# Optimization experiments

Measured on AMD Instinct MI355X. Metric: run time of the kernel, lower is better.

## Reference

```python
import jax, jax.numpy as jnp
import numpy as np

IN_CH = 64
HIDDEN_CH = 256

def setup_inputs() -> dict:
    key = jax.random.key(0)
    k = jax.random.split(key, 8)
    za = jax.random.normal(k[0], (8, 256, IN_CH), dtype=jnp.float32)
    zb = jax.random.normal(k[1], (8, 256, IN_CH), dtype=jnp.float32)
    # 1x1 conv weights stored as (out_ch, in_ch); biases zero per torch init
    w0 = jax.random.normal(k[2], (HIDDEN_CH, IN_CH), dtype=jnp.float32) * 0.05
    b0 = jnp.zeros((HIDDEN_CH,), dtype=jnp.float32)
    w1 = jax.random.normal(k[3], (HIDDEN_CH, HIDDEN_CH), dtype=jnp.float32) * 0.05
    b1 = jnp.zeros((HIDDEN_CH,), dtype=jnp.float32)
    w2 = jax.random.normal(k[4], (1, HIDDEN_CH), dtype=jnp.float32) * 0.05
    b2 = jnp.zeros((1,), dtype=jnp.float32)
    return {"za": za, "zb": zb, "w0": w0, "b0": b0, "w1": w1, "b1": b1, "w2": w2, "b2": b2}

def _leaky_relu(x):
    return jnp.where(x >= 0, x, 0.01 * x)  # torch LeakyReLU default slope

def reference(za, zb, w0, b0, w1, b1, w2, b2):
    # z_dif: (N, A, B, C) pairwise broadcast difference (channel-last; 1x1 conv = per-pixel linear)
    z_dif = za[:, :, None, :] - zb[:, None, :, :]
    y = _leaky_relu(jnp.einsum('nabc,hc->nabh', z_dif, w0) + b0)
    y = _leaky_relu(jnp.einsum('nabh,gh->nabg', y, w1) + b1)
    y = jax.nn.sigmoid(jnp.einsum('nabh,oh->nabo', y, w2) + b2)
    return y[..., 0]  # (N, A, B)
```

## Files before the change

### kernel.cpp

```cpp
#include <hip/hip_runtime.h>


typedef float f32x16 __attribute__((ext_vector_type(16)));
typedef short bf16x8 __attribute__((ext_vector_type(8)));

static __device__ __forceinline__ unsigned short f32_to_bf16(float f) {
    unsigned int u = __float_as_uint(f);
    u += 0x7FFFu + ((u >> 16) & 1u);
    return (unsigned short)(u >> 16);
}
static __device__ __forceinline__ float bf16_to_f32(unsigned short s) {
    return __uint_as_float(((unsigned int)s) << 16);
}

__global__ __launch_bounds__(256) void pack_uv_kernel(
    const float* __restrict__ za, const float* __restrict__ zb,
    const float* __restrict__ w0, const float* __restrict__ b0,
    unsigned short* __restrict__ upack, unsigned short* __restrict__ vpack) {
  int bid = blockIdx.x;
  int which = bid >> 11;
  int nr = bid & 2047;
  int n = nr >> 8, r = nr & 255;
  const float* z = (which ? zb : za) + nr * 64;
  __shared__ float zrow[64];
  int tid = threadIdx.x;
  if (tid < 64) zrow[tid] = z[tid];
  __syncthreads();
  int h = tid;
  const float* w0r = w0 + h * 64;
  float acc = 0.f;
#pragma unroll
  for (int c = 0; c < 64; c += 4) {
    float4 w = *reinterpret_cast<const float4*>(w0r + c);
    acc += w.x * zrow[c] + w.y * zrow[c + 1] + w.z * zrow[c + 2] + w.w * zrow[c + 3];
  }
  if (which == 0) {
    acc += b0[h];
    upack[nr * 256 + h] = f32_to_bf16(acc);
  } else {
    int bblock = r >> 5, lcol = r & 31;
    int kiter = h >> 4, rem = h & 15, half = rem >> 3, j = rem & 7;
    int lane = half * 32 + lcol;
    vpack[(((n * 8 + bblock) * 16 + kiter) * 64 + lane) * 8 + j] = f32_to_bf16(acc);
  }
}

__global__ __launch_bounds__(256) void pack_w1_kernel(
    const float* __restrict__ w1, unsigned short* __restrict__ w1pk) {
  int id = blockIdx.x * 256 + threadIdx.x;
  int g = id >> 8, h = id & 255;
  float val = w1[id];
  int nb = g >> 5, lcol = g & 31;
  int kiter = h >> 4, rem = h & 15, half = rem >> 3, j = rem & 7;
  int lane = half * 32 + lcol;
  w1pk[((kiter * 8 + nb) * 64 + lane) * 8 + j] = f32_to_bf16(val);
}

__global__ __launch_bounds__(512, 2) void fused_main_kernel(
    const unsigned short* __restrict__ upack,
    const unsigned short* __restrict__ vpack,
    const unsigned short* __restrict__ w1pk,
    const float* __restrict__ b1, const float* __restrict__ w2,
    const float* __restrict__ b2, float* __restrict__ out) {
  __shared__ __align__(16) unsigned short lwb[32768];
  int bid = blockIdx.x;
  int n = bid >> 8;
  int tid = threadIdx.x;
  int wid = tid >> 6;
  int l = tid & 63;
  int l31 = l & 31, lh = l >> 5;

  f32x16 acc[8];
#pragma unroll
  for (int cf = 0; cf < 8; ++cf)
#pragma unroll
    for (int r = 0; r < 16; ++r) acc[cf][r] = 0.f;

  float b1v[8], w2v[8];
#pragma unroll
  for (int cf = 0; cf < 8; ++cf) {
    b1v[cf] = b1[cf * 32 + l31];
    w2v[cf] = w2[cf * 32 + l31];
  }

  const bf16x8* vp8 = reinterpret_cast<const bf16x8*>(vpack);
  const unsigned short* ub = upack + bid * 256;
  const bf16x8* w1p8 = reinterpret_cast<const bf16x8*>(w1pk);
  bf16x8* lwb8 = reinterpret_cast<bf16x8*>(lwb);

  int vbase = ((n * 8 + wid) * 16) * 64 + l;

  for (int khalf = 0; khalf < 2; ++khalf) {
    __syncthreads();
#pragma unroll
    for (int it = 0; it < 8; ++it) {
      int cid = it * 512 + tid;
      lwb8[cid] = w1p8[khalf * 4096 + cid];
    }
    __syncthreads();

    bf16x8 afrag[8];
#pragma unroll
    for (int kk = 0; kk < 8; ++kk) {
      int kiter = khalf * 8 + kk;
      bf16x8 vv = vp8[vbase + kiter * 64];
      bf16x8 uu = *reinterpret_cast<const bf16x8*>(ub + kiter * 16 + lh * 8);
#pragma unroll
      for (int j = 0; j < 8; ++j) {
        float d = bf16_to_f32((unsigned short)uu[j]) - bf16_to_f32((unsigned short)vv[j]);
        d = fmaxf(d, 0.01f * d);
        afrag[kk][j] = (short)f32_to_bf16(d);
      }
    }

#pragma unroll
    for (int kk = 0; kk < 8; ++kk) {
#pragma unroll
      for (int cf = 0; cf < 8; ++cf) {
        bf16x8 bfrag = lwb8[(kk * 8 + cf) * 64 + l];
        acc[cf] = __builtin_amdgcn_mfma_f32_32x32x16_bf16(afrag[kk], bfrag, acc[cf], 0, 0, 0);
      }
    }
  }

  float p[16];
#pragma unroll
  for (int r = 0; r < 16; ++r) p[r] = 0.f;
#pragma unroll
  for (int cf = 0; cf < 8; ++cf) {
#pragma unroll
    for (int r = 0; r < 16; ++r) {
      float h1 = acc[cf][r] + b1v[cf];
      h1 = fmaxf(h1, 0.01f * h1);
      p[r] += h1 * w2v[cf];
    }
  }
#pragma unroll
  for (int r = 0; r < 16; ++r) {
#pragma unroll
    for (int m = 1; m < 32; m <<= 1) p[r] += __shfl_xor(p[r], m, 64);
  }
  float b2v = b2[0];
  if (l31 == 0) {
    int obase = bid * 256 + wid * 32 + 4 * lh;
#pragma unroll
    for (int r = 0; r < 16; ++r) {
      int row = (r & 3) + 8 * (r >> 2);
      out[obase + row] = 1.f / (1.f + __expf(-(p[r] + b2v)));
    }
  }
}

extern "C" void kernel_launch(void* const* d_in, const int* in_sizes, int n_in,
                              void* d_out, int out_size, void* d_ws, size_t ws_size,
                              hipStream_t stream) {
  const float* za = (const float*)d_in[0];
  const float* zb = (const float*)d_in[1];
  const float* w0 = (const float*)d_in[2];
  const float* b0 = (const float*)d_in[3];
  const float* w1 = (const float*)d_in[4];
  const float* b1 = (const float*)d_in[5];
  const float* w2 = (const float*)d_in[6];
  const float* b2 = (const float*)d_in[7];
  float* out = (float*)d_out;

  char* ws = (char*)d_ws;
  unsigned short* upack = (unsigned short*)ws;
  unsigned short* vpack = (unsigned short*)(ws + (1u << 20));
  unsigned short* w1pk  = (unsigned short*)(ws + (2u << 20));

  pack_uv_kernel<<<4096, 256, 0, stream>>>(za, zb, w0, b0, upack, vpack);
  pack_w1_kernel<<<256, 256, 0, stream>>>(w1, w1pk);
  fused_main_kernel<<<2048, 512, 0, stream>>>(upack, vpack, w1pk, b1, w2, b2, out);
}
```

Measured before the change: 163.1 us.

## Process two A rows per block with full W1 in LDS via direct global-to-LDS loads

The main kernel now gives each 256-thread block two A rows and half the B columns, so every B fragment read from LDS feeds two MFMAs. All of W1 (128 KB) is staged into LDS at once using global_load_lds, with a 64 KB two-phase fallback if the larger allocation is refused. U and V are kept in fp32 and converted to bf16 only after the subtraction, which improves accuracy but doubles their global traffic. The pack kernel also computes the za and zb projections in one launch. The cost is one block per CU, which limits latency hiding, and higher register use from two accumulator sets.

```diff
diff --git a/kernel.cpp b/kernel.cpp
--- a/kernel.cpp
+++ b/kernel.cpp
@@ -5,44 +5,36 @@
 typedef short bf16x8 __attribute__((ext_vector_type(8)));
 
 static __device__ __forceinline__ unsigned short f32_to_bf16(float f) {
-    unsigned int u = __float_as_uint(f);
-    u += 0x7FFFu + ((u >> 16) & 1u);
-    return (unsigned short)(u >> 16);
-}
-static __device__ __forceinline__ float bf16_to_f32(unsigned short s) {
-    return __uint_as_float(((unsigned int)s) << 16);
+  unsigned int u = __float_as_uint(f);
+  u += 0x7FFFu + ((u >> 16) & 1u);
+  return (unsigned short)(u >> 16);
 }
 
 __global__ __launch_bounds__(256) void pack_uv_kernel(
     const float* __restrict__ za, const float* __restrict__ zb,
     const float* __restrict__ w0, const float* __restrict__ b0,
-    unsigned short* __restrict__ upack, unsigned short* __restrict__ vpack) {
-  int bid = blockIdx.x;
-  int which = bid >> 11;
-  int nr = bid & 2047;
+    float* __restrict__ upack, float* __restrict__ vpack) {
+  int nr = blockIdx.x;
   int n = nr >> 8, r = nr & 255;
-  const float* z = (which ? zb : za) + nr * 64;
-  __shared__ float zrow[64];
+  __shared__ float arow[64], brow[64];
   int tid = threadIdx.x;
-  if (tid < 64) zrow[tid] = z[tid];
+  if (tid < 64) arow[tid] = za[nr * 64 + tid];
+  else if (tid < 128) brow[tid - 64] = zb[nr * 64 + (tid - 64)];
   __syncthreads();
   int h = tid;
   const float* w0r = w0 + h * 64;
-  float acc = 0.f;
+  float ua = 0.f, vb = 0.f;
 #pragma unroll
   for (int c = 0; c < 64; c += 4) {
     float4 w = *reinterpret_cast<const float4*>(w0r + c);
-    acc += w.x * zrow[c] + w.y * zrow[c + 1] + w.z * zrow[c + 2] + w.w * zrow[c + 3];
+    ua += w.x * arow[c] + w.y * arow[c + 1] + w.z * arow[c + 2] + w.w * arow[c + 3];
+    vb += w.x * brow[c] + w.y * brow[c + 1] + w.z * brow[c + 2] + w.w * brow[c + 3];
   }
-  if (which == 0) {
-    acc += b0[h];
-    upack[nr * 256 + h] = f32_to_bf16(acc);
-  } else {
-    int bblock = r >> 5, lcol = r & 31;
-    int kiter = h >> 4, rem = h & 15, half = rem >> 3, j = rem & 7;
-    int lane = half * 32 + lcol;
-    vpack[(((n * 8 + bblock) * 16 + kiter) * 64 + lane) * 8 + j] = f32_to_bf16(acc);
-  }
+  upack[nr * 256 + h] = ua + b0[h];
+  int bblock = r >> 5, lcol = r & 31;
+  int kiter = h >> 4, rem = h & 15, half = rem >> 3, j = rem & 7;
+  int lane = half * 32 + lcol;
+  vpack[(((n * 8 + bblock) * 16 + kiter) * 64 + lane) * 8 + j] = vb;
 }
 
 __global__ __launch_bounds__(256) void pack_w1_kernel(
@@ -56,25 +48,29 @@
   w1pk[((kiter * 8 + nb) * 64 + lane) * 8 + j] = f32_to_bf16(val);
 }
 
-__global__ __launch_bounds__(512, 2) void fused_main_kernel(
-    const unsigned short* __restrict__ upack,
-    const unsigned short* __restrict__ vpack,
+template <int KCHUNK>
+__global__ __launch_bounds__(256, 1) void fused_main(
+    const float* __restrict__ upack, const float* __restrict__ vpack,
     const unsigned short* __restrict__ w1pk,
     const float* __restrict__ b1, const float* __restrict__ w2,
     const float* __restrict__ b2, float* __restrict__ out) {
-  __shared__ __align__(16) unsigned short lwb[32768];
+  extern __shared__ __align__(16) unsigned char lds_raw[];
   int bid = blockIdx.x;
   int n = bid >> 8;
+  int apair = (bid >> 1) & 127;
+  int bhalf = bid & 1;
+  int a0 = apair * 2, a1 = a0 + 1;
   int tid = threadIdx.x;
   int wid = tid >> 6;
   int l = tid & 63;
   int l31 = l & 31, lh = l >> 5;
+  int bblk = bhalf * 4 + wid;
 
-  f32x16 acc[8];
+  f32x16 acc0[8], acc1[8];
 #pragma unroll
   for (int cf = 0; cf < 8; ++cf)
 #pragma unroll
-    for (int r = 0; r < 16; ++r) acc[cf][r] = 0.f;
+    for (int r = 0; r < 16; ++r) { acc0[cf][r] = 0.f; acc1[cf][r] = 0.f; }
 
   float b1v[8], w2v[8];
 #pragma unroll
@@ -83,70 +79,88 @@
     w2v[cf] = w2[cf * 32 + l31];
   }
 
-  const bf16x8* vp8 = reinterpret_cast<const bf16x8*>(vpack);
-  const unsigned short* ub = upack + bid * 256;
-  const bf16x8* w1p8 = reinterpret_cast<const bf16x8*>(w1pk);
-  bf16x8* lwb8 = reinterpret_cast<bf16x8*>(lwb);
+  const bf16x8* lfrag = reinterpret_cast<const bf16x8*>(lds_raw);
+  const int nphase = 16 / KCHUNK;
 
-  int vbase = ((n * 8 + wid) * 16) * 64 + l;
-
-  for (int khalf = 0; khalf < 2; ++khalf) {
-    __syncthreads();
+  for (int ph = 0; ph < nphase; ++ph) {
+    if (ph) __syncthreads();
+    const unsigned char* gsrc =
+        reinterpret_cast<const unsigned char*>(w1pk) + ph * KCHUNK * 8192;
 #pragma unroll
-    for (int it = 0; it < 8; ++it) {
-      int cid = it * 512 + tid;
-      lwb8[cid] = w1p8[khalf * 4096 + cid];
+    for (int it = 0; it < KCHUNK * 2; ++it) {
+      int chunk = it * 4 + wid;
+      __builtin_amdgcn_global_load_lds(
+          (const __attribute__((address_space(1))) void*)(gsrc + chunk * 1024 + l * 16),
+          (__attribute__((address_space(3))) void*)(lds_raw + chunk * 1024),
+          16, 0, 0);
     }
     __syncthreads();
 
-    bf16x8 afrag[8];
+    const float* vb = vpack + ((size_t)((n * 8 + bblk) * 16 + ph * KCHUNK)) * 512 + l * 8;
+    const float* u0b = upack + (n * 256 + a0) * 256 + ph * KCHUNK * 16 + lh * 8;
+    const float* u1b = upack + (n * 256 + a1) * 256 + ph * KCHUNK * 16 + lh * 8;
+
 #pragma unroll
-    for (int kk = 0; kk < 8; ++kk) {
-      int kiter = khalf * 8 + kk;
-      bf16x8 vv = vp8[vbase + kiter * 64];
-      bf16x8 uu = *reinterpret_cast<const bf16x8*>(ub + kiter * 16 + lh * 8);
+    for (int kk = 0; kk < KCHUNK; ++kk) {
+      float4 vA = *reinterpret_cast<const float4*>(vb + kk * 512);
+      float4 vB = *reinterpret_cast<const float4*>(vb + kk * 512 + 4);
+      float4 uA0 = *reinterpret_cast<const float4*>(u0b + kk * 16);
+      float4 uA1 = *reinterpret_cast<const float4*>(u0b + kk * 16 + 4);
+      float4 uB0 = *reinterpret_cast<const float4*>(u1b + kk * 16);
+      float4 uB1 = *reinterpret_cast<const float4*>(u1b + kk * 16 + 4);
+      float vv[8] = {vA.x, vA.y, vA.z, vA.w, vB.x, vB.y, vB.z, vB.w};
+      float u0[8] = {uA0.x, uA0.y, uA0.z, uA0.w, uA1.x, uA1.y, uA1.z, uA1.w};
+      float u1[8] = {uB0.x, uB0.y, uB0.z, uB0.w, uB1.x, uB1.y, uB1.z, uB1.w};
+      bf16x8 af0, af1;
 #pragma unroll
       for (int j = 0; j < 8; ++j) {
-        float d = bf16_to_f32((unsigned short)uu[j]) - bf16_to_f32((unsigned short)vv[j]);
-        d = fmaxf(d, 0.01f * d);
-        afrag[kk][j] = (short)f32_to_bf16(d);
+        float d0 = u0[j] - vv[j];
+        d0 = fmaxf(d0, 0.01f * d0);
+        af0[j] = (short)f32_to_bf16(d0);
+        float d1 = u1[j] - vv[j];
+        d1 = fmaxf(d1, 0.01f * d1);
+        af1[j] = (short)f32_to_bf16(d1);
       }
-    }
-
-#pragma unroll
-    for (int kk = 0; kk < 8; ++kk) {
 #pragma unroll
       for (int cf = 0; cf < 8; ++cf) {
-        bf16x8 bfrag = lwb8[(kk * 8 + cf) * 64 + l];
-        acc[cf] = __builtin_amdgcn_mfma_f32_32x32x16_bf16(afrag[kk], bfrag, acc[cf], 0, 0, 0);
+        bf16x8 bf = lfrag[(kk * 8 + cf) * 64 + l];
+        acc0[cf] = __builtin_amdgcn_mfma_f32_32x32x16_bf16(af0, bf, acc0[cf], 0, 0, 0);
+        acc1[cf] = __builtin_amdgcn_mfma_f32_32x32x16_bf16(af1, bf, acc1[cf], 0, 0, 0);
       }
     }
   }
 
-  float p[16];
+  float p0[16], p1[16];
 #pragma unroll
-  for (int r = 0; r < 16; ++r) p[r] = 0.f;
+  for (int r = 0; r < 16; ++r) { p0[r] = 0.f; p1[r] = 0.f; }
 #pragma unroll
   for (int cf = 0; cf < 8; ++cf) {
 #pragma unroll
     for (int r = 0; r < 16; ++r) {
-      float h1 = acc[cf][r] + b1v[cf];
+      float h0 = acc0[cf][r] + b1v[cf];
+      h0 = fmaxf(h0, 0.01f * h0);
+      p0[r] += h0 * w2v[cf];
+      float h1 = acc1[cf][r] + b1v[cf];
       h1 = fmaxf(h1, 0.01f * h1);
-      p[r] += h1 * w2v[cf];
+      p1[r] += h1 * w2v[cf];
     }
   }
 #pragma unroll
   for (int r = 0; r < 16; ++r) {
 #pragma unroll
-    for (int m = 1; m < 32; m <<= 1) p[r] += __shfl_xor(p[r], m, 64);
+    for (int m = 1; m < 32; m <<= 1) {
+      p0[r] += __shfl_xor(p0[r], m, 64);
+      p1[r] += __shfl_xor(p1[r], m, 64);
+    }
   }
   float b2v = b2[0];
   if (l31 == 0) {
-    int obase = bid * 256 + wid * 32 + 4 * lh;
+    int bcol = bhalf * 128 + wid * 32 + 4 * lh;
 #pragma unroll
     for (int r = 0; r < 16; ++r) {
       int row = (r & 3) + 8 * (r >> 2);
-      out[obase + row] = 1.f / (1.f + __expf(-(p[r] + b2v)));
+      out[(n * 256 + a0) * 256 + bcol + row] = 1.f / (1.f + __expf(-(p0[r] + b2v)));
+      out[(n * 256 + a1) * 256 + bcol + row] = 1.f / (1.f + __expf(-(p1[r] + b2v)));
     }
   }
 }
@@ -165,11 +179,19 @@
   float* out = (float*)d_out;
 
   char* ws = (char*)d_ws;
-  unsigned short* upack = (unsigned short*)ws;
-  unsigned short* vpack = (unsigned short*)(ws + (1u << 20));
-  unsigned short* w1pk  = (unsigned short*)(ws + (2u << 20));
+  float* upack = (float*)ws;
+  float* vpack = (float*)(ws + (2u << 20));
+  unsigned short* w1pk = (unsigned short*)(ws + (4u << 20));
 
-  pack_uv_kernel<<<4096, 256, 0, stream>>>(za, zb, w0, b0, upack, vpack);
+  pack_uv_kernel<<<2048, 256, 0, stream>>>(za, zb, w0, b0, upack, vpack);
   pack_w1_kernel<<<256, 256, 0, stream>>>(w1, w1pk);
-  fused_main_kernel<<<2048, 512, 0, stream>>>(upack, vpack, w1pk, b1, w2, b2, out);
+
+  hipError_t e = hipFuncSetAttribute(
+      reinterpret_cast<const void*>(fused_main<16>),
+      hipFuncAttributeMaxDynamicSharedMemorySize, 131072);
+  if (e == hipSuccess) {
+    fused_main<16><<<2048, 256, 131072, stream>>>(upack, vpack, w1pk, b1, w2, b2, out);
+  } else {
+    fused_main<8><<<2048, 256, 65536, stream>>>(upack, vpack, w1pk, b1, w2, b2, out);
+  }
 }
```

Measured after the change: 166.7 us. 1.02x slower.

## Keep W1 in registers, switch to fp16 packed math, restructure main kernel tiling

Applied to the files above, without the earlier changes.

The main kernel now holds each wave's slice of W1 as fp16 MFMA fragments in registers for the whole block and loops over 32 rows of A. This replaces reloading W1 into shared memory per block. The pairwise difference and LeakyReLU are computed with packed fp16 vector ops instead of per-element bf16/fp32 conversions, and the bias is folded into the accumulator init. The u/v packing is merged into one launch with half the blocks. Risks are the heavy register use for the W1 fragments, a per-row __syncthreads for the cross-wave reduction, and a different numerical precision.

```diff
diff --git a/kernel.cpp b/kernel.cpp
--- a/kernel.cpp
+++ b/kernel.cpp
@@ -1,152 +1,128 @@
 #include <hip/hip_runtime.h>
+#include <hip/hip_fp16.h>
 
 
 typedef float f32x16 __attribute__((ext_vector_type(16)));
-typedef short bf16x8 __attribute__((ext_vector_type(8)));
-
-static __device__ __forceinline__ unsigned short f32_to_bf16(float f) {
-    unsigned int u = __float_as_uint(f);
-    u += 0x7FFFu + ((u >> 16) & 1u);
-    return (unsigned short)(u >> 16);
-}
-static __device__ __forceinline__ float bf16_to_f32(unsigned short s) {
-    return __uint_as_float(((unsigned int)s) << 16);
-}
+typedef _Float16 f16x8 __attribute__((ext_vector_type(8)));
 
 __global__ __launch_bounds__(256) void pack_uv_kernel(
     const float* __restrict__ za, const float* __restrict__ zb,
     const float* __restrict__ w0, const float* __restrict__ b0,
-    unsigned short* __restrict__ upack, unsigned short* __restrict__ vpack) {
-  int bid = blockIdx.x;
-  int which = bid >> 11;
-  int nr = bid & 2047;
+    _Float16* __restrict__ upack, _Float16* __restrict__ vpack) {
+  int nr = blockIdx.x;
   int n = nr >> 8, r = nr & 255;
-  const float* z = (which ? zb : za) + nr * 64;
-  __shared__ float zrow[64];
+  __shared__ float arow[64], brow[64];
   int tid = threadIdx.x;
-  if (tid < 64) zrow[tid] = z[tid];
+  if (tid < 64) arow[tid] = za[nr * 64 + tid];
+  else if (tid < 128) brow[tid - 64] = zb[nr * 64 + (tid - 64)];
   __syncthreads();
   int h = tid;
   const float* w0r = w0 + h * 64;
-  float acc = 0.f;
+  float ua = 0.f, vb = 0.f;
 #pragma unroll
   for (int c = 0; c < 64; c += 4) {
     float4 w = *reinterpret_cast<const float4*>(w0r + c);
-    acc += w.x * zrow[c] + w.y * zrow[c + 1] + w.z * zrow[c + 2] + w.w * zrow[c + 3];
+    ua += w.x * arow[c] + w.y * arow[c + 1] + w.z * arow[c + 2] + w.w * arow[c + 3];
+    vb += w.x * brow[c] + w.y * brow[c + 1] + w.z * brow[c + 2] + w.w * brow[c + 3];
   }
-  if (which == 0) {
-    acc += b0[h];
-    upack[nr * 256 + h] = f32_to_bf16(acc);
-  } else {
-    int bblock = r >> 5, lcol = r & 31;
-    int kiter = h >> 4, rem = h & 15, half = rem >> 3, j = rem & 7;
-    int lane = half * 32 + lcol;
-    vpack[(((n * 8 + bblock) * 16 + kiter) * 64 + lane) * 8 + j] = f32_to_bf16(acc);
-  }
+  upack[nr * 256 + h] = (_Float16)(ua + b0[h]);
+  int bblk = r >> 5, lcol = r & 31;
+  int kiter = h >> 4, rem = h & 15, lh = rem >> 3, j = rem & 7;
+  int lane = lh * 32 + lcol;
+  vpack[(((n * 8 + bblk) * 16 + kiter) * 64 + lane) * 8 + j] = (_Float16)vb;
 }
 
 __global__ __launch_bounds__(256) void pack_w1_kernel(
-    const float* __restrict__ w1, unsigned short* __restrict__ w1pk) {
+    const float* __restrict__ w1, _Float16* __restrict__ w1pk) {
   int id = blockIdx.x * 256 + threadIdx.x;
-  int g = id >> 8, h = id & 255;
-  float val = w1[id];
-  int nb = g >> 5, lcol = g & 31;
-  int kiter = h >> 4, rem = h & 15, half = rem >> 3, j = rem & 7;
-  int lane = half * 32 + lcol;
-  w1pk[((kiter * 8 + nb) * 64 + lane) * 8 + j] = f32_to_bf16(val);
+  int g = id >> 8, k = id & 255;
+  int gt = g >> 5, lcol = g & 31;
+  int kiter = k >> 4, rem = k & 15, lh = rem >> 3, j = rem & 7;
+  int lane = lh * 32 + lcol;
+  w1pk[((kiter * 8 + gt) * 64 + lane) * 8 + j] = (_Float16)w1[id];
 }
 
-__global__ __launch_bounds__(512, 2) void fused_main_kernel(
-    const unsigned short* __restrict__ upack,
-    const unsigned short* __restrict__ vpack,
-    const unsigned short* __restrict__ w1pk,
+__global__ __launch_bounds__(256, 2) void fused_main(
+    const _Float16* __restrict__ upack, const _Float16* __restrict__ vpack,
+    const _Float16* __restrict__ w1pk,
     const float* __restrict__ b1, const float* __restrict__ w2,
     const float* __restrict__ b2, float* __restrict__ out) {
-  __shared__ __align__(16) unsigned short lwb[32768];
+  __shared__ float lds_p[2][4][32];
   int bid = blockIdx.x;
-  int n = bid >> 8;
+  int n = bid >> 6;
+  int bblk = (bid >> 3) & 7;
+  int aoct = bid & 7;
   int tid = threadIdx.x;
-  int wid = tid >> 6;
+  int ws = tid >> 6;
   int l = tid & 63;
   int l31 = l & 31, lh = l >> 5;
 
-  f32x16 acc[8];
+  f16x8 w1f[16][2];
 #pragma unroll
-  for (int cf = 0; cf < 8; ++cf)
+  for (int kt = 0; kt < 16; ++kt) {
 #pragma unroll
-    for (int r = 0; r < 16; ++r) acc[cf][r] = 0.f;
+    for (int t = 0; t < 2; ++t) {
+      int gt = 2 * ws + t;
+      w1f[kt][t] = *reinterpret_cast<const f16x8*>(w1pk + ((kt * 8 + gt) * 64 + l) * 8);
+    }
+  }
+  f32x16 b1acc[2];
+#pragma unroll
+  for (int t = 0; t < 2; ++t) {
+#pragma unroll
+    for (int rg = 0; rg < 4; ++rg) {
+      float4 bb = *reinterpret_cast<const float4*>(b1 + (2 * ws + t) * 32 + 8 * rg + 4 * lh);
+      b1acc[t][rg * 4 + 0] = bb.x;
+      b1acc[t][rg * 4 + 1] = bb.y;
+      b1acc[t][rg * 4 + 2] = bb.z;
+      b1acc[t][rg * 4 + 3] = bb.w;
+    }
+  }
+  float b2v = b2[0];
 
-  float b1v[8], w2v[8];
+  const _Float16 c001 = (_Float16)0.01f;
+  const f16x8 c001v = {c001, c001, c001, c001, c001, c001, c001, c001};
+
+  const _Float16* vb = vpack + (size_t)((n * 8 + bblk) * 16) * 512 + l * 8;
+
+  for (int it = 0; it < 32; ++it) {
+    int a = aoct * 32 + it;
+    const _Float16* ur = upack + (size_t)(n * 256 + a) * 256 + lh * 8;
+
+    f32x16 acc[2];
+    acc[0] = b1acc[0];
+    acc[1] = b1acc[1];
+
 #pragma unroll
-  for (int cf = 0; cf < 8; ++cf) {
-    b1v[cf] = b1[cf * 32 + l31];
-    w2v[cf] = w2[cf * 32 + l31];
-  }
+    for (int kt = 0; kt < 16; ++kt) {
+      f16x8 uu = *reinterpret_cast<const f16x8*>(ur + kt * 16);
+      f16x8 vv = *reinterpret_cast<const f16x8*>(vb + kt * 512);
+      f16x8 d = uu - vv;
+      f16x8 r = __builtin_elementwise_max(d, d * c001v);
+      acc[0] = __builtin_amdgcn_mfma_f32_32x32x16_f16(w1f[kt][0], r, acc[0], 0, 0, 0);
+      acc[1] = __builtin_amdgcn_mfma_f32_32x32x16_f16(w1f[kt][1], r, acc[1], 0, 0, 0);
+    }
 
-  const bf16x8* vp8 = reinterpret_cast<const bf16x8*>(vpack);
-  const unsigned short* ub = upack + bid * 256;
-  const bf16x8* w1p8 = reinterpret_cast<const bf16x8*>(w1pk);
-  bf16x8* lwb8 = reinterpret_cast<bf16x8*>(lwb);
-
-  int vbase = ((n * 8 + wid) * 16) * 64 + l;
-
-  for (int khalf = 0; khalf < 2; ++khalf) {
-    __syncthreads();
+    float p = 0.f;
 #pragma unroll
-    for (int it = 0; it < 8; ++it) {
-      int cid = it * 512 + tid;
-      lwb8[cid] = w1p8[khalf * 4096 + cid];
-    }
-    __syncthreads();
-
-    bf16x8 afrag[8];
+    for (int t = 0; t < 2; ++t) {
 #pragma unroll
-    for (int kk = 0; kk < 8; ++kk) {
-      int kiter = khalf * 8 + kk;
-      bf16x8 vv = vp8[vbase + kiter * 64];
-      bf16x8 uu = *reinterpret_cast<const bf16x8*>(ub + kiter * 16 + lh * 8);
-#pragma unroll
-      for (int j = 0; j < 8; ++j) {
-        float d = bf16_to_f32((unsigned short)uu[j]) - bf16_to_f32((unsigned short)vv[j]);
-        d = fmaxf(d, 0.01f * d);
-        afrag[kk][j] = (short)f32_to_bf16(d);
+      for (int rg = 0; rg < 4; ++rg) {
+        float4 ww = *reinterpret_cast<const float4*>(w2 + (2 * ws + t) * 32 + 8 * rg + 4 * lh);
+        float h0 = acc[t][rg * 4 + 0]; h0 = fmaxf(h0, 0.01f * h0); p = fmaf(h0, ww.x, p);
+        float h1 = acc[t][rg * 4 + 1]; h1 = fmaxf(h1, 0.01f * h1); p = fmaf(h1, ww.y, p);
+        float h2 = acc[t][rg * 4 + 2]; h2 = fmaxf(h2, 0.01f * h2); p = fmaf(h2, ww.z, p);
+        float h3 = acc[t][rg * 4 + 3]; h3 = fmaxf(h3, 0.01f * h3); p = fmaf(h3, ww.w, p);
       }
     }
+    p += __shfl_xor(p, 32, 64);
 
-#pragma unroll
-    for (int kk = 0; kk < 8; ++kk) {
-#pragma unroll
-      for (int cf = 0; cf < 8; ++cf) {
-        bf16x8 bfrag = lwb8[(kk * 8 + cf) * 64 + l];
-        acc[cf] = __builtin_amdgcn_mfma_f32_32x32x16_bf16(afrag[kk], bfrag, acc[cf], 0, 0, 0);
-      }
-    }
-  }
-
-  float p[16];
-#pragma unroll
-  for (int r = 0; r < 16; ++r) p[r] = 0.f;
-#pragma unroll
-  for (int cf = 0; cf < 8; ++cf) {
-#pragma unroll
-    for (int r = 0; r < 16; ++r) {
-      float h1 = acc[cf][r] + b1v[cf];
-      h1 = fmaxf(h1, 0.01f * h1);
-      p[r] += h1 * w2v[cf];
-    }
-  }
-#pragma unroll
-  for (int r = 0; r < 16; ++r) {
-#pragma unroll
-    for (int m = 1; m < 32; m <<= 1) p[r] += __shfl_xor(p[r], m, 64);
-  }
-  float b2v = b2[0];
-  if (l31 == 0) {
-    int obase = bid * 256 + wid * 32 + 4 * lh;
-#pragma unroll
-    for (int r = 0; r < 16; ++r) {
-      int row = (r & 3) + 8 * (r >> 2);
-      out[obase + row] = 1.f / (1.f + __expf(-(p[r] + b2v)));
+    int ph = it & 1;
+    if (l < 32) lds_p[ph][ws][l] = p;
+    __syncthreads();
+    if (ws == 0 && l < 32) {
+      float s = lds_p[ph][0][l] + lds_p[ph][1][l] + lds_p[ph][2][l] + lds_p[ph][3][l] + b2v;
+      out[(size_t)(n * 256 + a) * 256 + bblk * 32 + l] = 1.f / (1.f + __expf(-s));
     }
   }
 }
@@ -165,11 +141,11 @@
   float* out = (float*)d_out;
 
   char* ws = (char*)d_ws;
-  unsigned short* upack = (unsigned short*)ws;
-  unsigned short* vpack = (unsigned short*)(ws + (1u << 20));
-  unsigned short* w1pk  = (unsigned short*)(ws + (2u << 20));
+  _Float16* upack = (_Float16*)ws;
+  _Float16* vpack = (_Float16*)(ws + (1u << 20));
+  _Float16* w1pk  = (_Float16*)(ws + (2u << 20));
 
-  pack_uv_kernel<<<4096, 256, 0, stream>>>(za, zb, w0, b0, upack, vpack);
+  pack_uv_kernel<<<2048, 256, 0, stream>>>(za, zb, w0, b0, upack, vpack);
   pack_w1_kernel<<<256, 256, 0, stream>>>(w1, w1pk);
-  fused_main_kernel<<<2048, 512, 0, stream>>>(upack, vpack, w1pk, b1, w2, b2, out);
+  fused_main<<<512, 256, 0, stream>>>(upack, vpack, w1pk, b1, w2, b2, out);
 }
```

After: 214.0 us. 1.31x slower.
